# Performance work log

Hardware: AMD Instinct MI355X
Metric: run time of the kernel (lower is better)

Reference implementation:

```python
import jax, jax.numpy as jnp
import numpy as np

B = 262144
MA = [128, 128]
MB = [128, 128]


def krone_linear(x_a, x_b, wa, wb, ba, bb):
    # slice inputs to each branch's in_features (torch slices the wider branch)
    ia, ib = wa.shape[1], wb.shape[1]
    x_a = x_a[:, :ia]
    x_b = x_b[:, :ib]
    h_a = x_a @ wa.T + ba
    h_b = x_b @ wb.T + bb
    # zero-pad the narrower output so both branches share a width (static shapes)
    oa, ob = wa.shape[0], wb.shape[0]
    if oa > ob:
        h_b = jnp.pad(h_b, ((0, 0), (0, oa - ob)))
    elif ob > oa:
        h_a = jnp.pad(h_a, ((0, 0), (0, ob - oa)))
    return h_a, h_b


def krone_softmax(x_a, x_b, fa, fb):
    x_a = x_a[:, :fa]
    x_b = x_b[:, :fb]
    # vectorized per-row Kronecker product: kron(a, b)[i*fb + j] = a[i]*b[j]
    y = (x_a[:, :, None] * x_b[:, None, :]).reshape(x_a.shape[0], fa * fb)
    return jax.nn.softmax(y, axis=1)


def setup_inputs() -> dict:
    key = jax.random.key(0)
    ks = jax.random.split(key, 13)
    s = 0.1
    inp = {
        "x": jax.random.normal(ks[0], (2, B, 2), dtype=jnp.float32),
        "w1a": jax.random.normal(ks[1], (MA[0], 2), dtype=jnp.float32) * s,
        "w1b": jax.random.normal(ks[2], (MB[0], 2), dtype=jnp.float32) * s,
        "b1a": jax.random.normal(ks[3], (MA[0],), dtype=jnp.float32) * s,
        "b1b": jax.random.normal(ks[4], (MB[0],), dtype=jnp.float32) * s,
        "w2a": jax.random.normal(ks[5], (MA[1], MA[0]), dtype=jnp.float32) * s,
        "w2b": jax.random.normal(ks[6], (MB[1], MB[0]), dtype=jnp.float32) * s,
        "b2a": jax.random.normal(ks[7], (MA[1],), dtype=jnp.float32) * s,
        "b2b": jax.random.normal(ks[8], (MB[1],), dtype=jnp.float32) * s,
        "w3a": jax.random.normal(ks[9], (1, MA[1]), dtype=jnp.float32) * s,
        "w3b": jax.random.normal(ks[10], (3, MB[1]), dtype=jnp.float32) * s,
        "b3a": jax.random.normal(ks[11], (1,), dtype=jnp.float32) * s,
        "b3b": jax.random.normal(ks[12], (3,), dtype=jnp.float32) * s,
    }
    return inp


def reference(x, w1a, w1b, b1a, b1b, w2a, w2b, b2a, b2b, w3a, w3b, b3a, b3b):
    x_a, x_b = x[0], x[1]
    h_a, h_b = krone_linear(x_a, x_b, w1a, w1b, b1a, b1b)
    h_a, h_b = jax.nn.relu(h_a), jax.nn.relu(h_b)
    h_a, h_b = krone_linear(h_a, h_b, w2a, w2b, b2a, b2b)
    h_a, h_b = jax.nn.relu(h_a), jax.nn.relu(h_b)
    h_a, h_b = krone_linear(h_a, h_b, w3a, w3b, b3a, b3b)
    return krone_softmax(h_a, h_b, 1, 3)
```

## Files before the change

kernel.cpp:

```cpp
#include <hip/hip_runtime.h>
#include <hip/hip_bf16.h>


#define BTOT 262144
#define NBLK (BTOT / 256)

typedef __attribute__((ext_vector_type(4))) float floatx4;
typedef __attribute__((ext_vector_type(8))) short bf16x8;
typedef __attribute__((ext_vector_type(4))) int  intx4;

#define OFF_W2  0
#define OFF_W1  32768
#define OFF_B2  35072
#define OFF_W3  35584
#define OFF_SA  37120
#define LDS_TOTAL 38144

static __device__ __forceinline__ int pack2bf(float lo, float hi) {
    unsigned a = __builtin_bit_cast(unsigned, lo) + 0x8000u;
    unsigned b = __builtin_bit_cast(unsigned, hi) + 0x8000u;
    return (int)__builtin_amdgcn_perm(b, a, 0x07060302u);
}

#define SEL4(a0, a1, a2, a3, i) \
    ((i) == 0 ? (a0) : (i) == 1 ? (a1) : (i) == 2 ? (a2) : (a3))

static __device__ __forceinline__ float redcol(float v) {
    v += __shfl_xor(v, 1); v += __shfl_xor(v, 2);
    v += __shfl_xor(v, 4); v += __shfl_xor(v, 8);
    return v;
}

static __device__ __forceinline__ int w1slot(int k) { return k + (k >> 3); }

static __device__ __forceinline__ void pack_path(
        unsigned char* smem, int tid,
        const float* __restrict__ w2, const float* __restrict__ w1,
        const float* __restrict__ b1, const float* __restrict__ b2) {
    const float4* w2p = (const float4*)w2;
    #pragma unroll
    for (int i = 0; i < 16; ++i) {
        int u = i * 256 + tid;
        int n = u >> 5;
        float4 f = w2p[u];
        int k = (u & 31) * 4;
        int s = k >> 5;
        int j0 = k & 7;
        int l = ((k & 31) >> 3) * 16 + (n & 15);
        int2 pkd;
        pkd.x = pack2bf(f.x, f.y);
        pkd.y = pack2bf(f.z, f.w);
        *(int2*)(smem + OFF_W2 + (s * 8 + (n >> 4)) * 1024 + l * 16 + j0 * 2) = pkd;
    }
    if (tid < 128) {
        ((float4*)(smem + OFF_W1))[w1slot(tid)] =
            make_float4(w1[2 * tid], w1[2 * tid + 1], b1[tid], 0.f);
        ((float*)(smem + OFF_B2))[tid] = b2[tid];
    }
}

#define GEMM_CHUNK(acc, XV, W1p, W2p, B2p)                                     \
    {                                                                          \
        _Pragma("unroll")                                                      \
        for (int t = 0; t < 8; ++t) {                                          \
            float b2n = (B2p)[t * 16 + col];                                   \
            floatx4 bi = (floatx4){b2n, b2n, b2n, b2n};                        \
            _Pragma("unroll")                                                  \
            for (int mt = 0; mt < 2; ++mt) acc[t][mt] = bi;                    \
        }                                                                      \
        _Pragma("unroll")                                                      \
        for (int s = 0; s < 4; ++s) {                                          \
            intx4 af[2];                                                       \
            const int bslot = s * 36 + quad * 9;                               \
            _Pragma("unroll")                                                  \
            for (int j2 = 0; j2 < 4; ++j2) {                                   \
                float4 c0 = (W1p)[bslot + 2 * j2];                             \
                float4 c1 = (W1p)[bslot + 2 * j2 + 1];                         \
                _Pragma("unroll")                                              \
                for (int mt = 0; mt < 2; ++mt) {                               \
                    float h0 = fmaxf(fmaf((XV)[mt].x, c0.x,                    \
                                fmaf((XV)[mt].y, c0.y, c0.z)), 0.f);           \
                    float h1 = fmaxf(fmaf((XV)[mt].x, c1.x,                    \
                                fmaf((XV)[mt].y, c1.y, c1.z)), 0.f);           \
                    af[mt][j2] = pack2bf(h0, h1);                              \
                }                                                              \
            }                                                                  \
            _Pragma("unroll")                                                  \
            for (int t = 0; t < 8; ++t) {                                      \
                bf16x8 bfr = (W2p)[(s * 8 + t) * 64 + lane];                   \
                _Pragma("unroll")                                              \
                for (int mt = 0; mt < 2; ++mt)                                 \
                    acc[t][mt] = __builtin_amdgcn_mfma_f32_16x16x32_bf16(      \
                        __builtin_bit_cast(bf16x8, af[mt]), bfr,               \
                        acc[t][mt], 0, 0, 0);                                  \
            }                                                                  \
        }                                                                      \
    }

__global__ __launch_bounds__(256, 2)
void krone_fused(const float* __restrict__ x,
                 const float* __restrict__ w1a, const float* __restrict__ w1b,
                 const float* __restrict__ b1a, const float* __restrict__ b1b,
                 const float* __restrict__ w2a, const float* __restrict__ w2b,
                 const float* __restrict__ b2a, const float* __restrict__ b2b,
                 const float* __restrict__ w3a, const float* __restrict__ w3b,
                 const float* __restrict__ b3a, const float* __restrict__ b3b,
                 float* __restrict__ out) {
    __shared__ __align__(16) unsigned char smem[LDS_TOTAL];

    const int tid  = threadIdx.x;
    const int lane = tid & 63;
    const int wave = tid >> 6;
    const int quad = lane >> 4;
    const int col  = lane & 15;

    const float2* xA = (const float2*)x;
    const float2* xB = xA + BTOT;
    float2 xa[4], xb[4];
    #pragma unroll
    for (int c = 0; c < 2; ++c)
        #pragma unroll
        for (int mt = 0; mt < 2; ++mt) {
            int idx = blockIdx.x * 256 + c * 128 + wave * 32 + mt * 16 + col;
            xa[c * 2 + mt] = xA[idx];
            xb[c * 2 + mt] = xB[idx];
        }
    const float b3a_ = b3a[0];
    const float b30 = b3b[0], b31 = b3b[1], b32 = b3b[2];

    const bf16x8* W2 = (const bf16x8*)(smem + OFF_W2);
    const float4* W1 = (const float4*)(smem + OFF_W1);
    const float*  B2 = (const float*)(smem + OFF_B2);
    const float*  W3 = (const float*)(smem + OFF_W3);
    float*        SA = (float*)(smem + OFF_SA);

    pack_path(smem, tid, w2a, w1a, b1a, b2a);
    if (tid < 128) ((float*)(smem + OFF_W3))[tid] = w3a[tid];
    __syncthreads();

    #pragma unroll
    for (int c = 0; c < 2; ++c) {
        __builtin_amdgcn_sched_barrier(0);
        floatx4 acc[8][2];
        GEMM_CHUNK(acc, xa + 2 * c, W1, W2, B2);
        __builtin_amdgcn_sched_barrier(0);

        float pa[2][4] = {};
        #pragma unroll
        for (int t = 0; t < 8; ++t) {
            float w3n = W3[t * 16 + col];
            #pragma unroll
            for (int mt = 0; mt < 2; ++mt)
                #pragma unroll
                for (int r = 0; r < 4; ++r)
                    pa[mt][r] = fmaf(w3n, fmaxf(acc[t][mt][r], 0.f), pa[mt][r]);
        }
        #pragma unroll
        for (int mt = 0; mt < 2; ++mt)
            #pragma unroll
            for (int r = 0; r < 4; ++r) pa[mt][r] = redcol(pa[mt][r]);
        __builtin_amdgcn_sched_barrier(0);

        if (col < 4) {
            #pragma unroll
            for (int mt = 0; mt < 2; ++mt) {
                int sl = mt * 16 + quad * 4 + col;
                SA[c * 128 + wave * 32 + sl] =
                    SEL4(pa[mt][0], pa[mt][1], pa[mt][2], pa[mt][3], col) + b3a_;
            }
        }
        __builtin_amdgcn_sched_barrier(0);
    }

    __syncthreads();
    pack_path(smem, tid, w2b, w1b, b1b, b2b);
    for (int i = tid; i < 384; i += 256) ((float*)(smem + OFF_W3))[i] = w3b[i];
    __syncthreads();

    #pragma unroll
    for (int c = 0; c < 2; ++c) {
        __builtin_amdgcn_sched_barrier(0);
        floatx4 acc[8][2];
        GEMM_CHUNK(acc, xb + 2 * c, W1, W2, B2);
        __builtin_amdgcn_sched_barrier(0);

        float p0[2][4] = {}, p1[2][4] = {}, p2[2][4] = {};
        #pragma unroll
        for (int t = 0; t < 8; ++t) {
            int n = t * 16 + col;
            float w30 = W3[n], w31 = W3[128 + n], w32 = W3[256 + n];
            #pragma unroll
            for (int mt = 0; mt < 2; ++mt)
                #pragma unroll
                for (int r = 0; r < 4; ++r) {
                    float h = fmaxf(acc[t][mt][r], 0.f);
                    p0[mt][r] = fmaf(w30, h, p0[mt][r]);
                    p1[mt][r] = fmaf(w31, h, p1[mt][r]);
                    p2[mt][r] = fmaf(w32, h, p2[mt][r]);
                }
        }
        #pragma unroll
        for (int mt = 0; mt < 2; ++mt)
            #pragma unroll
            for (int r = 0; r < 4; ++r) {
                p0[mt][r] = redcol(p0[mt][r]);
                p1[mt][r] = redcol(p1[mt][r]);
                p2[mt][r] = redcol(p2[mt][r]);
            }
        __builtin_amdgcn_sched_barrier(0);

        if (col < 4) {
            #pragma unroll
            for (int mt = 0; mt < 2; ++mt) {
                int sl = mt * 16 + quad * 4 + col;
                float t0 = SEL4(p0[mt][0], p0[mt][1], p0[mt][2], p0[mt][3], col) + b30;
                float t1 = SEL4(p1[mt][0], p1[mt][1], p1[mt][2], p1[mt][3], col) + b31;
                float t2 = SEL4(p2[mt][0], p2[mt][1], p2[mt][2], p2[mt][3], col) + b32;
                float sa = SA[c * 128 + wave * 32 + sl];
                float y0 = sa * t0, y1 = sa * t1, y2 = sa * t2;
                float m = fmaxf(y0, fmaxf(y1, y2));
                float e0 = __expf(y0 - m), e1 = __expf(y1 - m), e2 = __expf(y2 - m);
                float rs = 1.f / (e0 + e1 + e2);
                long o = (long)(blockIdx.x * 256 + c * 128 + wave * 32 + sl) * 3;
                out[o]     = e0 * rs;
                out[o + 1] = e1 * rs;
                out[o + 2] = e2 * rs;
            }
        }
        __builtin_amdgcn_sched_barrier(0);
    }
}

extern "C" void kernel_launch(void* const* d_in, const int* in_sizes, int n_in,
                              void* d_out, int out_size, void* d_ws, size_t ws_size,
                              hipStream_t stream) {
    const float* x   = (const float*)d_in[0];
    const float* w1a = (const float*)d_in[1];
    const float* w1b = (const float*)d_in[2];
    const float* b1a = (const float*)d_in[3];
    const float* b1b = (const float*)d_in[4];
    const float* w2a = (const float*)d_in[5];
    const float* w2b = (const float*)d_in[6];
    const float* b2a = (const float*)d_in[7];
    const float* b2b = (const float*)d_in[8];
    const float* w3a = (const float*)d_in[9];
    const float* w3b = (const float*)d_in[10];
    const float* b3a = (const float*)d_in[11];
    const float* b3b = (const float*)d_in[12];
    float* out = (float*)d_out;

    krone_fused<<<NBLK, 256, 0, stream>>>(x, w1a, w1b, b1a, b1b, w2a, w2b,
                                          b2a, b2b, w3a, w3b, b3a, b3b, out);
}
```

Before: 119.9 us.

## Use 512-thread blocks with one x buffer and per-tile epilogue

Blocks grow to 512 threads (8 waves) covering 512 rows, so each block packs the branch weights into LDS once for twice as many rows. Each wave now owns a contiguous 64-row slab. The kernel keeps a single x register buffer, loading branch-B inputs only after branch A finishes. The branch-B epilogue is processed one m-tile at a time to lower register pressure, with launch bounds raised to 512x4. The weight-packing loop is remapped to 8 iterations over the larger thread count. The aim is to amortize weight staging and raise occupancy, at the cost of fewer blocks, heavier per-block barriers and possible register spills under the tighter launch bound.

```diff
diff --git a/kernel.cpp b/kernel.cpp
--- a/kernel.cpp
+++ b/kernel.cpp
@@ -3,7 +3,7 @@
 
 
 #define BTOT 262144
-#define NBLK (BTOT / 256)
+#define NBLK (BTOT / 512)
 
 typedef __attribute__((ext_vector_type(4))) float floatx4;
 typedef __attribute__((ext_vector_type(8))) short bf16x8;
@@ -14,7 +14,7 @@
 #define OFF_B2  35072
 #define OFF_W3  35584
 #define OFF_SA  37120
-#define LDS_TOTAL 38144
+#define LDS_TOTAL 39168
 
 static __device__ __forceinline__ int pack2bf(float lo, float hi) {
     unsigned a = __builtin_bit_cast(unsigned, lo) + 0x8000u;
@@ -39,11 +39,11 @@
         const float* __restrict__ b1, const float* __restrict__ b2) {
     const float4* w2p = (const float4*)w2;
     #pragma unroll
-    for (int i = 0; i < 16; ++i) {
-        int u = i * 256 + tid;
-        int n = u >> 5;
-        float4 f = w2p[u];
-        int k = (u & 31) * 4;
+    for (int i = 0; i < 8; ++i) {
+        int n  = (tid & 15) | (i << 4);
+        int k4 = tid >> 4;
+        float4 f = w2p[n * 32 + k4];
+        int k = k4 * 4;
         int s = k >> 5;
         int j0 = k & 7;
         int l = ((k & 31) >> 3) * 16 + (n & 15);
@@ -97,7 +97,7 @@
         }                                                                      \
     }
 
-__global__ __launch_bounds__(256, 2)
+__global__ __launch_bounds__(512, 4)
 void krone_fused(const float* __restrict__ x,
                  const float* __restrict__ w1a, const float* __restrict__ w1b,
                  const float* __restrict__ b1a, const float* __restrict__ b1b,
@@ -113,26 +113,25 @@
     const int wave = tid >> 6;
     const int quad = lane >> 4;
     const int col  = lane & 15;
-
-    const float2* xA = (const float2*)x;
-    const float2* xB = xA + BTOT;
-    float2 xa[4], xb[4];
-    #pragma unroll
-    for (int c = 0; c < 2; ++c)
-        #pragma unroll
-        for (int mt = 0; mt < 2; ++mt) {
-            int idx = blockIdx.x * 256 + c * 128 + wave * 32 + mt * 16 + col;
-            xa[c * 2 + mt] = xA[idx];
-            xb[c * 2 + mt] = xB[idx];
-        }
-    const float b3a_ = b3a[0];
-    const float b30 = b3b[0], b31 = b3b[1], b32 = b3b[2];
+    const int wbase = blockIdx.x * 512 + wave * 64;
 
     const bf16x8* W2 = (const bf16x8*)(smem + OFF_W2);
     const float4* W1 = (const float4*)(smem + OFF_W1);
     const float*  B2 = (const float*)(smem + OFF_B2);
     const float*  W3 = (const float*)(smem + OFF_W3);
     float*        SA = (float*)(smem + OFF_SA);
+    const float2* xA = (const float2*)x;
+    const float2* xB = xA + BTOT;
+
+    const float b3a_ = b3a[0];
+    const float b30 = b3b[0], b31 = b3b[1], b32 = b3b[2];
+
+    float2 xv[4];
+    #pragma unroll
+    for (int c = 0; c < 2; ++c)
+        #pragma unroll
+        for (int mt = 0; mt < 2; ++mt)
+            xv[c * 2 + mt] = xA[wbase + c * 32 + mt * 16 + col];
 
     pack_path(smem, tid, w2a, w1a, b1a, b2a);
     if (tid < 128) ((float*)(smem + OFF_W3))[tid] = w3a[tid];
@@ -142,7 +141,7 @@
     for (int c = 0; c < 2; ++c) {
         __builtin_amdgcn_sched_barrier(0);
         floatx4 acc[8][2];
-        GEMM_CHUNK(acc, xa + 2 * c, W1, W2, B2);
+        GEMM_CHUNK(acc, xv + 2 * c, W1, W2, B2);
         __builtin_amdgcn_sched_barrier(0);
 
         float pa[2][4] = {};
@@ -165,63 +164,63 @@
             #pragma unroll
             for (int mt = 0; mt < 2; ++mt) {
                 int sl = mt * 16 + quad * 4 + col;
-                SA[c * 128 + wave * 32 + sl] =
+                SA[wave * 64 + c * 32 + sl] =
                     SEL4(pa[mt][0], pa[mt][1], pa[mt][2], pa[mt][3], col) + b3a_;
             }
         }
         __builtin_amdgcn_sched_barrier(0);
     }
+
+    #pragma unroll
+    for (int c = 0; c < 2; ++c)
+        #pragma unroll
+        for (int mt = 0; mt < 2; ++mt)
+            xv[c * 2 + mt] = xB[wbase + c * 32 + mt * 16 + col];
 
     __syncthreads();
     pack_path(smem, tid, w2b, w1b, b1b, b2b);
-    for (int i = tid; i < 384; i += 256) ((float*)(smem + OFF_W3))[i] = w3b[i];
+    if (tid < 384) ((float*)(smem + OFF_W3))[tid] = w3b[tid];
     __syncthreads();
 
     #pragma unroll
     for (int c = 0; c < 2; ++c) {
         __builtin_amdgcn_sched_barrier(0);
         floatx4 acc[8][2];
-        GEMM_CHUNK(acc, xb + 2 * c, W1, W2, B2);
-        __builtin_amdgcn_sched_barrier(0);
-
-        float p0[2][4] = {}, p1[2][4] = {}, p2[2][4] = {};
-        #pragma unroll
-        for (int t = 0; t < 8; ++t) {
-            int n = t * 16 + col;
-            float w30 = W3[n], w31 = W3[128 + n], w32 = W3[256 + n];
-            #pragma unroll
-            for (int mt = 0; mt < 2; ++mt)
+        GEMM_CHUNK(acc, xv + 2 * c, W1, W2, B2);
+        __builtin_amdgcn_sched_barrier(0);
+
+        #pragma unroll
+        for (int mt = 0; mt < 2; ++mt) {
+            float p0[4] = {}, p1[4] = {}, p2[4] = {};
+            #pragma unroll
+            for (int t = 0; t < 8; ++t) {
+                int n = t * 16 + col;
+                float w30 = W3[n], w31 = W3[128 + n], w32 = W3[256 + n];
                 #pragma unroll
                 for (int r = 0; r < 4; ++r) {
                     float h = fmaxf(acc[t][mt][r], 0.f);
-                    p0[mt][r] = fmaf(w30, h, p0[mt][r]);
-                    p1[mt][r] = fmaf(w31, h, p1[mt][r]);
-                    p2[mt][r] = fmaf(w32, h, p2[mt][r]);
+                    p0[r] = fmaf(w30, h, p0[r]);
+                    p1[r] = fmaf(w31, h, p1[r]);
+                    p2[r] = fmaf(w32, h, p2[r]);
                 }
-        }
-        #pragma unroll
-        for (int mt = 0; mt < 2; ++mt)
+            }
             #pragma unroll
             for (int r = 0; r < 4; ++r) {
-                p0[mt][r] = redcol(p0[mt][r]);
-                p1[mt][r] = redcol(p1[mt][r]);
-                p2[mt][r] = redcol(p2[mt][r]);
-            }
-        __builtin_amdgcn_sched_barrier(0);
-
-        if (col < 4) {
-            #pragma unroll
-            for (int mt = 0; mt < 2; ++mt) {
+                p0[r] = redcol(p0[r]);
+                p1[r] = redcol(p1[r]);
+                p2[r] = redcol(p2[r]);
+            }
+            if (col < 4) {
                 int sl = mt * 16 + quad * 4 + col;
-                float t0 = SEL4(p0[mt][0], p0[mt][1], p0[mt][2], p0[mt][3], col) + b30;
-                float t1 = SEL4(p1[mt][0], p1[mt][1], p1[mt][2], p1[mt][3], col) + b31;
-                float t2 = SEL4(p2[mt][0], p2[mt][1], p2[mt][2], p2[mt][3], col) + b32;
-                float sa = SA[c * 128 + wave * 32 + sl];
+                float t0 = SEL4(p0[0], p0[1], p0[2], p0[3], col) + b30;
+                float t1 = SEL4(p1[0], p1[1], p1[2], p1[3], col) + b31;
+                float t2 = SEL4(p2[0], p2[1], p2[2], p2[3], col) + b32;
+                float sa = SA[wave * 64 + c * 32 + sl];
                 float y0 = sa * t0, y1 = sa * t1, y2 = sa * t2;
                 float m = fmaxf(y0, fmaxf(y1, y2));
                 float e0 = __expf(y0 - m), e1 = __expf(y1 - m), e2 = __expf(y2 - m);
                 float rs = 1.f / (e0 + e1 + e2);
-                long o = (long)(blockIdx.x * 256 + c * 128 + wave * 32 + sl) * 3;
+                long o = (long)(wbase + c * 32 + sl) * 3;
                 out[o]     = e0 * rs;
                 out[o + 1] = e1 * rs;
                 out[o + 2] = e2 * rs;
@@ -249,6 +248,6 @@
     const float* b3b = (const float*)d_in[12];
     float* out = (float*)d_out;
 
-    krone_fused<<<NBLK, 256, 0, stream>>>(x, w1a, w1b, b1a, b1b, w2a, w2b,
+    krone_fused<<<NBLK, 512, 0, stream>>>(x, w1a, w1b, b1a, b1b, w2a, w2b,
                                           b2a, b2b, w3a, w3b, b3a, b3b, out);
 }
```

New measurement: 111.2 us. -7.2%, faster.
